# Kernel optimization log

Hardware: AMD Instinct MI355X
Metric: run time of the kernel (lower is better)

Reference implementation:

```python
import jax, jax.numpy as jnp
import numpy as np

EMBED_DIM = 1024
NUM_HEADS = 16
HEAD_DIM = EMBED_DIM // NUM_HEADS
SCALE = HEAD_DIM ** -0.5


def setup_inputs() -> dict:
    key = jax.random.key(0)
    k_x, k_wqkv, k_bqkv, k_wo, k_bo = jax.random.split(key, 5)
    B, T, C = 2, 2048, EMBED_DIM
    bound = 1.0 / np.sqrt(C)
    return {
        "x": jax.random.normal(k_x, (B, T, C), dtype=jnp.float32),
        "w_qkv": jax.random.uniform(k_wqkv, (C, 3 * C), jnp.float32, -bound, bound),
        "b_qkv": jax.random.uniform(k_bqkv, (3 * C,), jnp.float32, -bound, bound),
        "w_out": jax.random.uniform(k_wo, (C, C), jnp.float32, -bound, bound),
        "b_out": jax.random.uniform(k_bo, (C,), jnp.float32, -bound, bound),
    }


def reference(x, w_qkv, b_qkv, w_out, b_out):
    B, T, C = x.shape
    H, D = NUM_HEADS, HEAD_DIM
    qkv = x @ w_qkv + b_qkv                      # [B,T,3C]
    q, k, v = jnp.split(qkv, 3, axis=-1)         # each [B,T,C]
    q = q.reshape(B, T, H, D).transpose(0, 2, 1, 3)  # [B,H,T,D]
    k = k.reshape(B, T, H, D).transpose(0, 2, 1, 3)
    v = v.reshape(B, T, H, D).transpose(0, 2, 1, 3)
    scores = jnp.einsum("bhqd,bhkd->bhqk", q, k) * SCALE  # [B,H,T,T]
    weights = jax.nn.softmax(scores, axis=-1)
    out = jnp.einsum("bhqk,bhkd->bhqd", weights, v)       # [B,H,T,D]
    concat = out.transpose(0, 2, 1, 3).reshape(B, T, C)
    return concat @ w_out + b_out
```

## Files before the change

kernel.cpp:

```cpp
#include <hip/hip_runtime.h>

typedef _Float16 f16;
typedef _Float16 f16x8 __attribute__((ext_vector_type(8)));
typedef _Float16 f16x4 __attribute__((ext_vector_type(4)));
typedef float f32x4 __attribute__((ext_vector_type(4)));
typedef float f32x16 __attribute__((ext_vector_type(16)));
typedef unsigned int u32x4 __attribute__((ext_vector_type(4)));

#define SCALE_Q (0.125f * 1.44269504088896f)

__device__ __forceinline__ f32x4 mfma16x16x32(f16x8 a, f16x8 b, f32x4 c) {
  return __builtin_amdgcn_mfma_f32_16x16x32_f16(a, b, c, 0, 0, 0);
}
__device__ __forceinline__ f32x16 mfma32x32x16(f16x8 a, f16x8 b, f32x16 c) {
  return __builtin_amdgcn_mfma_f32_32x32x16_f16(a, b, c, 0, 0, 0);
}

__device__ __forceinline__ float fexp2(float x) {
  float r;
  asm("v_exp_f32 %0, %1" : "=v"(r) : "v"(x));
  return r;
}

typedef const __attribute__((address_space(1))) void* gptr1;
typedef __attribute__((address_space(3))) void* lptr3;
__device__ __forceinline__ void gload_lds16(const void* g, void* l) {
  __builtin_amdgcn_global_load_lds((gptr1)g, (lptr3)l, 16, 0, 0);
}

__device__ __forceinline__ unsigned pk2(float a, float b) {
  return __builtin_bit_cast(unsigned, __builtin_amdgcn_cvt_pkrtz(a, b));
}

__global__ __launch_bounds__(256)
void cvt_f32_f16(const float* __restrict__ in, f16* __restrict__ out, int n4) {
  int i = blockIdx.x * 256 + threadIdx.x;
  if (i >= n4) return;
  float4 v = reinterpret_cast<const float4*>(in)[i];
  f16x4 o = {(f16)v.x, (f16)v.y, (f16)v.z, (f16)v.w};
  reinterpret_cast<f16x4*>(out)[i] = o;
}

__global__ __launch_bounds__(256)
void transpose_cvt(const float* __restrict__ in, f16* __restrict__ out, int R, int Cin) {
  __shared__ float tile[32][33];
  int bx = blockIdx.x * 32;
  int by = blockIdx.y * 32;
  int tx = threadIdx.x & 31, ty = threadIdx.x >> 5;
#pragma unroll
  for (int i = ty; i < 32; i += 8)
    tile[i][tx] = in[(size_t)(by + i) * Cin + bx + tx];
  __syncthreads();
#pragma unroll
  for (int i = ty; i < 32; i += 8)
    out[(size_t)(bx + i) * R + by + tx] = (f16)tile[tx][i];
}

__global__ __launch_bounds__(256)
void pack_kv(const f16* __restrict__ qkvh, f16* __restrict__ kP, f16* __restrict__ vP) {
  const int t64 = blockIdx.x;
  const int pair = blockIdx.y;
  const int b = pair >> 4, h = pair & 15;
  const f16* Ksrc = qkvh + (size_t)b * 2048 * 3072 + 1024 + h * 64;
  const f16* Vsrc = Ksrc + 1024;
  const int k0 = t64 * 64;
  const int tid = threadIdx.x;

#pragma unroll
  for (int c = 0; c < 2; ++c) {
    int u = tid + c * 256;
    int lane = u & 63;
    int kd = (u >> 6) & 3;
    int kt = u >> 8;
    int key = k0 + kt * 32 + (lane & 31);
    int dd = kd * 16 + (lane >> 5) * 8;
    f16x8 v = *reinterpret_cast<const f16x8*>(Ksrc + (size_t)key * 3072 + dd);
    *reinterpret_cast<f16x8*>(
        kP + ((((size_t)pair * 64 + t64 * 2 + kt) * 4 + kd) * 64 + lane) * 8) = v;
  }
#pragma unroll
  for (int c = 0; c < 2; ++c) {
    int u = tid + c * 256;
    int lane = u & 63;
    int r = u >> 6;
    int ks = r & 3, dhalf = r >> 2;
    int keyb = k0 + ks * 16 + (lane >> 5) * 8;
    int dd = dhalf * 32 + (lane & 31);
    f16x8 v;
#pragma unroll
    for (int j = 0; j < 8; ++j)
      v[j] = Vsrc[(size_t)(keyb + j) * 3072 + dd];
    *reinterpret_cast<f16x8*>(
        vP + ((((size_t)pair * 32 + t64) * 8 + r) * 64 + lane) * 8) = v;
  }
}

template<bool QKV_EPI>
__global__ __launch_bounds__(256)
void gemm_bt(const f16* __restrict__ A, const f16* __restrict__ Bt,
             const float* __restrict__ bias, f16* __restrict__ outh,
             float* __restrict__ outf, int M, int N, int K) {
  constexpr int BM = 128, BN = 128, BK = 32;
  __shared__ f16 As[BM * BK];
  __shared__ f16 Bs[BN * BK];
  const int tid = threadIdx.x;
  const int l = tid & 63;
  const int w = tid >> 6;
  const int wr = w >> 1, wc = w & 1;
  const int bm = blockIdx.x * BM, bn = blockIdx.y * BN;
  const int l15 = l & 15, lhi = l >> 4;

  f32x4 acc[4][4] = {};

  const char* Ab = (const char*)A;
  const char* Bb = (const char*)Bt;
  const size_t rowbytes = (size_t)K * 2;

  for (int kt = 0; kt < K; kt += BK) {
    __syncthreads();
#pragma unroll
    for (int c = 0; c < 2; ++c) {
      int o = tid * 16 + c * 4096;
      int r = o >> 6;
      int cb = o & 63;
      gload_lds16(Ab + (size_t)(bm + r) * rowbytes + (size_t)kt * 2 + cb, (char*)As + o);
      gload_lds16(Bb + (size_t)(bn + r) * rowbytes + (size_t)kt * 2 + cb, (char*)Bs + o);
    }
    __syncthreads();

    f16x8 af[4], bf[4];
#pragma unroll
    for (int i = 0; i < 4; ++i)
      af[i] = *reinterpret_cast<const f16x8*>(&As[(wr * 64 + i * 16 + l15) * BK + 8 * lhi]);
#pragma unroll
    for (int i = 0; i < 4; ++i)
      bf[i] = *reinterpret_cast<const f16x8*>(&Bs[(wc * 64 + i * 16 + l15) * BK + 8 * lhi]);
#pragma unroll
    for (int i = 0; i < 4; ++i)
#pragma unroll
      for (int j = 0; j < 4; ++j)
        acc[i][j] = mfma16x16x32(af[i], bf[j], acc[i][j]);
  }

#pragma unroll
  for (int i = 0; i < 4; ++i) {
#pragma unroll
    for (int j = 0; j < 4; ++j) {
      int gr0 = bm + wr * 64 + i * 16 + 4 * lhi;
      int gc = bn + wc * 64 + j * 16 + l15;
      float b = bias[gc];
#pragma unroll
      for (int r = 0; r < 4; ++r) {
        float v = acc[i][j][r] + b;
        if constexpr (QKV_EPI) {
          if (gc < 1024) v *= SCALE_Q;
          outh[(size_t)(gr0 + r) * N + gc] = (f16)v;
        } else {
          outf[(size_t)(gr0 + r) * N + gc] = v;
        }
      }
    }
  }
}

__global__ __launch_bounds__(256, 3)
void attn_kernel(const f16* __restrict__ qkv, const f16* __restrict__ kP,
                 const f16* __restrict__ vP, f16* __restrict__ outh) {
  constexpr int T = 2048;
  constexpr int ROW = 3072;
  __shared__ float mo[4096];
  __shared__ float MlBuf[2][64];

  const int tid = threadIdx.x;
  const int l = tid & 63;
  const int w = tid >> 6;
  const int wq = w >> 1;
  const int grp = w & 1;
  const int l31 = l & 31, hi = l >> 5;

  const int bid = blockIdx.x;
  const int pair = bid & 31;
  const int b = pair >> 4;
  const int h = pair & 15;
  const int qt = bid >> 5;

  const size_t base = (size_t)b * T * ROW;
  const int q0 = qt * 64 + wq * 32;

  f16x8 bq[4];
  {
    const f16* qp = qkv + base + (size_t)(q0 + l31) * ROW + h * 64 + hi * 8;
#pragma unroll
    for (int kd = 0; kd < 4; ++kd)
      bq[kd] = *reinterpret_cast<const f16x8*>(qp + kd * 16);
  }

  const f16* Kp = kP + (size_t)pair * 64 * 4 * 64 * 8;
  const f16* Vp = vP + (size_t)pair * 32 * 8 * 64 * 8;

  f32x16 o0 = {}, o1 = {};
  float l_r = 0.f;

  for (int t = 0; t < 16; ++t) {
    const int t64g = grp * 16 + t;
    const int t32g = t64g * 2;

    f16x8 ak[2][4];
#pragma unroll
    for (int kt = 0; kt < 2; ++kt)
#pragma unroll
      for (int kd = 0; kd < 4; ++kd)
        ak[kt][kd] = *reinterpret_cast<const f16x8*>(
            Kp + ((((size_t)t32g + kt) * 4 + kd) * 64 + l) * 8);

    f16x8 av0[4], av1[4];
#pragma unroll
    for (int ks = 0; ks < 4; ++ks) {
      av0[ks] = *reinterpret_cast<const f16x8*>(
          Vp + (((size_t)t64g * 8 + ks) * 64 + l) * 8);
      av1[ks] = *reinterpret_cast<const f16x8*>(
          Vp + (((size_t)t64g * 8 + 4 + ks) * 64 + l) * 8);
    }

    f32x16 s0 = {}, s1 = {};
    __builtin_amdgcn_s_setprio(1);
#pragma unroll
    for (int kd = 0; kd < 4; ++kd) s0 = mfma32x32x16(ak[0][kd], bq[kd], s0);
#pragma unroll
    for (int kd = 0; kd < 4; ++kd) s1 = mfma32x32x16(ak[1][kd], bq[kd], s1);
    __builtin_amdgcn_s_setprio(0);

    float sm[16];
#pragma unroll
    for (int r = 0; r < 16; ++r) {
      s0[r] = fexp2(s0[r]);
      s1[r] = fexp2(s1[r]);
      sm[r] = s0[r] + s1[r];
    }
#pragma unroll
    for (int st = 8; st > 0; st >>= 1)
#pragma unroll
      for (int r = 0; r < st; ++r) sm[r] += sm[r + st];
    l_r += sm[0] + __shfl_xor(sm[0], 32);

    f16x8 bp[4];
#pragma unroll
    for (int kt = 0; kt < 2; ++kt) {
#pragma unroll
      for (int s2 = 0; s2 < 2; ++s2) {
        u32x4 wd;
#pragma unroll
        for (int u = 0; u < 2; ++u) {
          float a0 = kt ? s1[8 * s2 + 2 * u] : s0[8 * s2 + 2 * u];
          float a1 = kt ? s1[8 * s2 + 2 * u + 1] : s0[8 * s2 + 2 * u + 1];
          float b0 = kt ? s1[8 * s2 + 4 + 2 * u] : s0[8 * s2 + 4 + 2 * u];
          float b1 = kt ? s1[8 * s2 + 4 + 2 * u + 1] : s0[8 * s2 + 4 + 2 * u + 1];
          unsigned wB = pk2(a0, a1);
          unsigned wA = pk2(b0, b1);
          unsigned oB = __shfl_xor(wB, 32);
          unsigned oA = __shfl_xor(wA, 32);
          wd[u]     = hi ? oA : wB;
          wd[2 + u] = hi ? wA : oB;
        }
        bp[2 * kt + s2] = __builtin_bit_cast(f16x8, wd);
      }
    }

    __builtin_amdgcn_s_setprio(1);
#pragma unroll
    for (int ks = 0; ks < 4; ++ks) {
      o0 = mfma32x32x16(av0[ks], bp[ks], o0);
      o1 = mfma32x32x16(av1[ks], bp[ks], o1);
    }
    __builtin_amdgcn_s_setprio(0);
  }

  const int mbase = wq * 2048 + l * 32;
  if (grp == 1) {
#pragma unroll
    for (int k = 0; k < 8; ++k) {
      int ks = k ^ (l & 7);
      f32x4 v;
      if (k < 4) { v = f32x4{o0[4*k], o0[4*k+1], o0[4*k+2], o0[4*k+3]}; }
      else       { int r = 4*(k-4); v = f32x4{o1[r], o1[r+1], o1[r+2], o1[r+3]}; }
      *reinterpret_cast<f32x4*>(&mo[mbase + ks * 4]) = v;
    }
    MlBuf[wq][l] = l_r;
  }
  __syncthreads();
  if (grp == 0) {
    float inv = 1.0f / (l_r + MlBuf[wq][l]);
    f16* orow = outh + (size_t)(b * T + q0 + l31) * 1024 + h * 64;
#pragma unroll
    for (int k = 0; k < 8; ++k) {
      int ks = k ^ (l & 7);
      f32x4 ob = *reinterpret_cast<const f32x4*>(&mo[mbase + ks * 4]);
#pragma unroll
      for (int j = 0; j < 4; ++j) {
        int r = 4 * (k & 3) + j;
        int d = (r & 3) + 8 * (r >> 2) + 4 * hi;
        float own = (k < 4) ? o0[r] : o1[r];
        float val = (own + ob[j]) * inv;
        orow[(k < 4 ? d : d + 32)] = (f16)val;
      }
    }
  }
}

extern "C" void kernel_launch(void* const* d_in, const int* in_sizes, int n_in,
                              void* d_out, int out_size, void* d_ws, size_t ws_size,
                              hipStream_t stream) {
  const float* x      = (const float*)d_in[0];
  const float* w_qkv  = (const float*)d_in[1];
  const float* b_qkv  = (const float*)d_in[2];
  const float* w_out  = (const float*)d_in[3];
  const float* b_out  = (const float*)d_in[4];
  float* out = (float*)d_out;

  char* ws = (char*)d_ws;
  f16* xh    = (f16*)(ws);
  f16* wqkvT = (f16*)(ws + 8388608);
  f16* qkvh  = (f16*)(ws + 16777216);
  f16* attnh = (f16*)(ws + 41943040);
  f16* kP    = (f16*)(ws);
  f16* vP    = (f16*)(ws + 8388608);
  f16* woutT = (f16*)(ws);

  cvt_f32_f16<<<4096, 256, 0, stream>>>(x, xh, 1048576);
  transpose_cvt<<<dim3(96, 32), 256, 0, stream>>>(w_qkv, wqkvT, 1024, 3072);
  gemm_bt<true><<<dim3(32, 24), 256, 0, stream>>>(xh, wqkvT, b_qkv, qkvh, nullptr,
                                                  4096, 3072, 1024);
  pack_kv<<<dim3(32, 32), 256, 0, stream>>>(qkvh, kP, vP);
  attn_kernel<<<1024, 256, 0, stream>>>(qkvh, kP, vP, attnh);
  transpose_cvt<<<dim3(32, 32), 256, 0, stream>>>(w_out, woutT, 1024, 1024);
  gemm_bt<false><<<dim3(32, 8), 256, 0, stream>>>(attnh, woutT, b_out, nullptr, out,
                                                  4096, 1024, 1024);
}
```

Baseline: 146.1 us.

## Stage K/V fragments through double-buffered LDS shared across query waves

The attention kernel no longer has each wave load its K and V fragments directly from global memory. Each key tile is now copied once per wave group into a double-buffered LDS area with direct global-to-LDS loads, so the two query waves in a group share it. The next tile is prefetched while the current one is computed, and the V fragment reads are moved after the softmax. The cost is a block-wide barrier every iteration, 64KB of LDS per block, and occupancy lowered from 3 to 2 blocks per CU; the old output-reduction buffers now reuse the same LDS space.

```diff
diff --git a/kernel.cpp b/kernel.cpp
--- a/kernel.cpp
+++ b/kernel.cpp
@@ -163,13 +163,12 @@
   }
 }
 
-__global__ __launch_bounds__(256, 3)
+__global__ __launch_bounds__(256, 2)
 void attn_kernel(const f16* __restrict__ qkv, const f16* __restrict__ kP,
                  const f16* __restrict__ vP, f16* __restrict__ outh) {
   constexpr int T = 2048;
   constexpr int ROW = 3072;
-  __shared__ float mo[4096];
-  __shared__ float MlBuf[2][64];
+  __shared__ f16 FragLds[2][2][8192];
 
   const int tid = threadIdx.x;
   const int l = tid & 63;
@@ -195,32 +194,40 @@
       bq[kd] = *reinterpret_cast<const f16x8*>(qp + kd * 16);
   }
 
-  const f16* Kp = kP + (size_t)pair * 64 * 4 * 64 * 8;
-  const f16* Vp = vP + (size_t)pair * 32 * 8 * 64 * 8;
+  const f16* Kp = kP + (size_t)pair * 131072;
+  const f16* Vp = vP + (size_t)pair * 131072;
+
+  const int sid8 = ((wq << 6) | l) * 8;
+
+#define STAGE(TG, BUF)                                                         \
+  do {                                                                         \
+    const f16* ks_ = Kp + (size_t)(TG) * 4096;                                 \
+    const f16* vs_ = Vp + (size_t)(TG) * 4096;                                 \
+    f16* db_ = &FragLds[grp][BUF][0];                                          \
+    _Pragma("unroll") for (int j = 0; j < 4; ++j)                              \
+      gload_lds16(ks_ + sid8 + j * 1024, db_ + sid8 + j * 1024);               \
+    _Pragma("unroll") for (int j = 0; j < 4; ++j)                              \
+      gload_lds16(vs_ + sid8 + j * 1024, db_ + 4096 + sid8 + j * 1024);        \
+  } while (0)
+
+  const int tbase = grp * 16;
+  STAGE(tbase, 0);
+  __syncthreads();
 
   f32x16 o0 = {}, o1 = {};
   float l_r = 0.f;
+  int buf = 0;
 
   for (int t = 0; t < 16; ++t) {
-    const int t64g = grp * 16 + t;
-    const int t32g = t64g * 2;
+    if (t < 15) STAGE(tbase + t + 1, buf ^ 1);
+    const f16* fb = &FragLds[grp][buf][0];
 
     f16x8 ak[2][4];
 #pragma unroll
     for (int kt = 0; kt < 2; ++kt)
 #pragma unroll
       for (int kd = 0; kd < 4; ++kd)
-        ak[kt][kd] = *reinterpret_cast<const f16x8*>(
-            Kp + ((((size_t)t32g + kt) * 4 + kd) * 64 + l) * 8);
-
-    f16x8 av0[4], av1[4];
-#pragma unroll
-    for (int ks = 0; ks < 4; ++ks) {
-      av0[ks] = *reinterpret_cast<const f16x8*>(
-          Vp + (((size_t)t64g * 8 + ks) * 64 + l) * 8);
-      av1[ks] = *reinterpret_cast<const f16x8*>(
-          Vp + (((size_t)t64g * 8 + 4 + ks) * 64 + l) * 8);
-    }
+        ak[kt][kd] = *reinterpret_cast<const f16x8*>(fb + ((kt * 4 + kd) * 64 + l) * 8);
 
     f32x16 s0 = {}, s1 = {};
     __builtin_amdgcn_s_setprio(1);
@@ -242,6 +249,13 @@
 #pragma unroll
       for (int r = 0; r < st; ++r) sm[r] += sm[r + st];
     l_r += sm[0] + __shfl_xor(sm[0], 32);
+
+    f16x8 av0[4], av1[4];
+#pragma unroll
+    for (int ks = 0; ks < 4; ++ks) {
+      av0[ks] = *reinterpret_cast<const f16x8*>(fb + 4096 + (ks * 64 + l) * 8);
+      av1[ks] = *reinterpret_cast<const f16x8*>(fb + 4096 + ((4 + ks) * 64 + l) * 8);
+    }
 
     f16x8 bp[4];
 #pragma unroll
@@ -273,8 +287,13 @@
       o1 = mfma32x32x16(av1[ks], bp[ks], o1);
     }
     __builtin_amdgcn_s_setprio(0);
-  }
-
+
+    __syncthreads();
+    buf ^= 1;
+  }
+
+  float* mo = reinterpret_cast<float*>(&FragLds[0][0][0]);
+  float* Ml = reinterpret_cast<float*>(&FragLds[1][0][0]);
   const int mbase = wq * 2048 + l * 32;
   if (grp == 1) {
 #pragma unroll
@@ -285,11 +304,11 @@
       else       { int r = 4*(k-4); v = f32x4{o1[r], o1[r+1], o1[r+2], o1[r+3]}; }
       *reinterpret_cast<f32x4*>(&mo[mbase + ks * 4]) = v;
     }
-    MlBuf[wq][l] = l_r;
+    Ml[wq * 64 + l] = l_r;
   }
   __syncthreads();
   if (grp == 0) {
-    float inv = 1.0f / (l_r + MlBuf[wq][l]);
+    float inv = 1.0f / (l_r + Ml[wq * 64 + l]);
     f16* orow = outh + (size_t)(b * T + q0 + l31) * 1024 + h * 64;
 #pragma unroll
     for (int k = 0; k < 8; ++k) {
@@ -305,6 +324,7 @@
       }
     }
   }
+#undef STAGE
 }
 
 extern "C" void kernel_launch(void* const* d_in, const int* in_sizes, int n_in,
```

Result: no change. 148.2 us (+1.5%).

## Fuse K/V packing into QKV GEMM epilogue and drop pack_kv kernel

Applied to the files above, without the earlier changes.

The QKV GEMM epilogue now writes Q into a compact scaled buffer and scatters K and V straight into the MFMA-friendly packed layouts the attention kernel reads. This removes the separate pack_kv launch and its extra read/write pass over K and V. The cost is scattered, less coalesced stores in the GEMM epilogue: K is written element by element and V in 4-wide chunks. The workspace layout changes so the packed buffers no longer alias xh and wqkvT, and the w_out transpose moves to run before attention.

```diff
diff --git a/kernel.cpp b/kernel.cpp
--- a/kernel.cpp
+++ b/kernel.cpp
@@ -57,49 +57,103 @@
 }
 
 __global__ __launch_bounds__(256)
-void pack_kv(const f16* __restrict__ qkvh, f16* __restrict__ kP, f16* __restrict__ vP) {
-  const int t64 = blockIdx.x;
-  const int pair = blockIdx.y;
-  const int b = pair >> 4, h = pair & 15;
-  const f16* Ksrc = qkvh + (size_t)b * 2048 * 3072 + 1024 + h * 64;
-  const f16* Vsrc = Ksrc + 1024;
-  const int k0 = t64 * 64;
+void gemm_qkv(const f16* __restrict__ A, const f16* __restrict__ Bt,
+              const float* __restrict__ bias, f16* __restrict__ qQ,
+              f16* __restrict__ kP, f16* __restrict__ vP) {
+  constexpr int BM = 128, BN = 128, BK = 32, K = 1024, N = 3072;
+  __shared__ f16 As[BM * BK];
+  __shared__ f16 Bs[BN * BK];
   const int tid = threadIdx.x;
-
-#pragma unroll
-  for (int c = 0; c < 2; ++c) {
-    int u = tid + c * 256;
-    int lane = u & 63;
-    int kd = (u >> 6) & 3;
-    int kt = u >> 8;
-    int key = k0 + kt * 32 + (lane & 31);
-    int dd = kd * 16 + (lane >> 5) * 8;
-    f16x8 v = *reinterpret_cast<const f16x8*>(Ksrc + (size_t)key * 3072 + dd);
-    *reinterpret_cast<f16x8*>(
-        kP + ((((size_t)pair * 64 + t64 * 2 + kt) * 4 + kd) * 64 + lane) * 8) = v;
-  }
-#pragma unroll
-  for (int c = 0; c < 2; ++c) {
-    int u = tid + c * 256;
-    int lane = u & 63;
-    int r = u >> 6;
-    int ks = r & 3, dhalf = r >> 2;
-    int keyb = k0 + ks * 16 + (lane >> 5) * 8;
-    int dd = dhalf * 32 + (lane & 31);
-    f16x8 v;
-#pragma unroll
-    for (int j = 0; j < 8; ++j)
-      v[j] = Vsrc[(size_t)(keyb + j) * 3072 + dd];
-    *reinterpret_cast<f16x8*>(
-        vP + ((((size_t)pair * 32 + t64) * 8 + r) * 64 + lane) * 8) = v;
-  }
-}
-
-template<bool QKV_EPI>
+  const int l = tid & 63;
+  const int w = tid >> 6;
+  const int wr = w >> 1, wc = w & 1;
+  const int bm = blockIdx.x * BM, bn = blockIdx.y * BN;
+  const int l15 = l & 15, lhi = l >> 4;
+
+  f32x4 acc[4][4] = {};
+
+  const char* Ab = (const char*)A;
+  const char* Bb = (const char*)Bt;
+  const size_t rowbytes = (size_t)K * 2;
+
+  for (int kt = 0; kt < K; kt += BK) {
+    __syncthreads();
+#pragma unroll
+    for (int c = 0; c < 2; ++c) {
+      int o = tid * 16 + c * 4096;
+      int r = o >> 6;
+      int cb = o & 63;
+      gload_lds16(Ab + (size_t)(bm + r) * rowbytes + (size_t)kt * 2 + cb, (char*)As + o);
+      gload_lds16(Bb + (size_t)(bn + r) * rowbytes + (size_t)kt * 2 + cb, (char*)Bs + o);
+    }
+    __syncthreads();
+
+    f16x8 af[4], bf[4];
+#pragma unroll
+    for (int i = 0; i < 4; ++i)
+      af[i] = *reinterpret_cast<const f16x8*>(&As[(wr * 64 + i * 16 + l15) * BK + 8 * lhi]);
+#pragma unroll
+    for (int i = 0; i < 4; ++i)
+      bf[i] = *reinterpret_cast<const f16x8*>(&Bs[(wc * 64 + i * 16 + l15) * BK + 8 * lhi]);
+#pragma unroll
+    for (int i = 0; i < 4; ++i)
+#pragma unroll
+      for (int j = 0; j < 4; ++j)
+        acc[i][j] = mfma16x16x32(af[i], bf[j], acc[i][j]);
+  }
+
+  const int region = bn >> 10;
+#pragma unroll
+  for (int i = 0; i < 4; ++i) {
+#pragma unroll
+    for (int j = 0; j < 4; ++j) {
+      int gr0 = bm + wr * 64 + i * 16 + 4 * lhi;
+      int gc = bn + wc * 64 + j * 16 + l15;
+      float bia = bias[gc];
+      if (region == 0) {
+#pragma unroll
+        for (int r = 0; r < 4; ++r) {
+          float v = (acc[i][j][r] + bia) * SCALE_Q;
+          qQ[(size_t)(gr0 + r) * 1024 + gc] = (f16)v;
+        }
+      } else if (region == 1) {
+        int dloc = gc - 1024;
+        int h = dloc >> 6, dd = dloc & 63;
+        int kd = dd >> 4, hi8 = (dd >> 3) & 1, j8 = dd & 7;
+        int bb = gr0 >> 11;
+        int pair = bb * 16 + h;
+#pragma unroll
+        for (int r = 0; r < 4; ++r) {
+          int key = (gr0 + r) & 2047;
+          int t32 = key >> 5, l31k = key & 31;
+          size_t idx = ((((size_t)pair * 64 + t32) * 4 + kd) * 64 + (hi8 * 32 + l31k)) * 8 + j8;
+          kP[idx] = (f16)(acc[i][j][r] + bia);
+        }
+      } else {
+        int dloc = gc - 2048;
+        int h = dloc >> 6, dd = dloc & 63;
+        int dhalf = dd >> 5, l31v = dd & 31;
+        int bb = gr0 >> 11;
+        int pair = bb * 16 + h;
+        int key = gr0 & 2047;
+        int t64 = key >> 6;
+        int k6 = key & 63;
+        int ks = k6 >> 4, hiv = (k6 >> 3) & 1, jv = k6 & 7;
+        int rr = dhalf * 4 + ks;
+        size_t idx = ((((size_t)pair * 32 + t64) * 8 + rr) * 64 + (hiv * 32 + l31v)) * 8 + jv;
+        f16x4 ov;
+#pragma unroll
+        for (int r = 0; r < 4; ++r) ov[r] = (f16)(acc[i][j][r] + bia);
+        *reinterpret_cast<f16x4*>(&vP[idx]) = ov;
+      }
+    }
+  }
+}
+
 __global__ __launch_bounds__(256)
-void gemm_bt(const f16* __restrict__ A, const f16* __restrict__ Bt,
-             const float* __restrict__ bias, f16* __restrict__ outh,
-             float* __restrict__ outf, int M, int N, int K) {
+void gemm_out(const f16* __restrict__ A, const f16* __restrict__ Bt,
+              const float* __restrict__ bias, float* __restrict__ outf,
+              int M, int N, int K) {
   constexpr int BM = 128, BN = 128, BK = 32;
   __shared__ f16 As[BM * BK];
   __shared__ f16 Bs[BN * BK];
@@ -150,24 +204,16 @@
       int gc = bn + wc * 64 + j * 16 + l15;
       float b = bias[gc];
 #pragma unroll
-      for (int r = 0; r < 4; ++r) {
-        float v = acc[i][j][r] + b;
-        if constexpr (QKV_EPI) {
-          if (gc < 1024) v *= SCALE_Q;
-          outh[(size_t)(gr0 + r) * N + gc] = (f16)v;
-        } else {
-          outf[(size_t)(gr0 + r) * N + gc] = v;
-        }
-      }
+      for (int r = 0; r < 4; ++r)
+        outf[(size_t)(gr0 + r) * N + gc] = acc[i][j][r] + b;
     }
   }
 }
 
 __global__ __launch_bounds__(256, 3)
-void attn_kernel(const f16* __restrict__ qkv, const f16* __restrict__ kP,
+void attn_kernel(const f16* __restrict__ qQ, const f16* __restrict__ kP,
                  const f16* __restrict__ vP, f16* __restrict__ outh) {
   constexpr int T = 2048;
-  constexpr int ROW = 3072;
   __shared__ float mo[4096];
   __shared__ float MlBuf[2][64];
 
@@ -184,19 +230,18 @@
   const int h = pair & 15;
   const int qt = bid >> 5;
 
-  const size_t base = (size_t)b * T * ROW;
   const int q0 = qt * 64 + wq * 32;
 
   f16x8 bq[4];
   {
-    const f16* qp = qkv + base + (size_t)(q0 + l31) * ROW + h * 64 + hi * 8;
+    const f16* qp = qQ + (size_t)(b * T + q0 + l31) * 1024 + h * 64 + hi * 8;
 #pragma unroll
     for (int kd = 0; kd < 4; ++kd)
       bq[kd] = *reinterpret_cast<const f16x8*>(qp + kd * 16);
   }
 
-  const f16* Kp = kP + (size_t)pair * 64 * 4 * 64 * 8;
-  const f16* Vp = vP + (size_t)pair * 32 * 8 * 64 * 8;
+  const f16* Kp = kP + (size_t)pair * 131072;
+  const f16* Vp = vP + (size_t)pair * 131072;
 
   f32x16 o0 = {}, o1 = {};
   float l_r = 0.f;
@@ -320,19 +365,16 @@
   char* ws = (char*)d_ws;
   f16* xh    = (f16*)(ws);
   f16* wqkvT = (f16*)(ws + 8388608);
-  f16* qkvh  = (f16*)(ws + 16777216);
+  f16* qQ    = (f16*)(ws + 16777216);
+  f16* kP    = (f16*)(ws + 25165824);
+  f16* vP    = (f16*)(ws + 33554432);
   f16* attnh = (f16*)(ws + 41943040);
-  f16* kP    = (f16*)(ws);
-  f16* vP    = (f16*)(ws + 8388608);
   f16* woutT = (f16*)(ws);
 
   cvt_f32_f16<<<4096, 256, 0, stream>>>(x, xh, 1048576);
   transpose_cvt<<<dim3(96, 32), 256, 0, stream>>>(w_qkv, wqkvT, 1024, 3072);
-  gemm_bt<true><<<dim3(32, 24), 256, 0, stream>>>(xh, wqkvT, b_qkv, qkvh, nullptr,
-                                                  4096, 3072, 1024);
-  pack_kv<<<dim3(32, 32), 256, 0, stream>>>(qkvh, kP, vP);
-  attn_kernel<<<1024, 256, 0, stream>>>(qkvh, kP, vP, attnh);
+  gemm_qkv<<<dim3(32, 24), 256, 0, stream>>>(xh, wqkvT, b_qkv, qQ, kP, vP);
   transpose_cvt<<<dim3(32, 32), 256, 0, stream>>>(w_out, woutT, 1024, 1024);
-  gemm_bt<false><<<dim3(32, 8), 256, 0, stream>>>(attnh, woutT, b_out, nullptr, out,
-                                                  4096, 1024, 1024);
-}
+  attn_kernel<<<1024, 256, 0, stream>>>(qQ, kP, vP, attnh);
+  gemm_out<<<dim3(32, 8), 256, 0, stream>>>(attnh, woutT, b_out, out, 4096, 1024, 1024);
+}
```

New measurement: 131.8 us. -9.8%, faster.
